# Kernel tuning notes

Hardware: AMD Instinct MI355X
Metric: run time of the kernel (lower is better)

Reference implementation:

```python
import jax, jax.numpy as jnp
import numpy as np

D_MODEL = 1024
Q_DIM = K_DIM = V_DIM = 1024
MASKED = True

def setup_inputs() -> dict:
    key = jax.random.key(0)
    ks = jax.random.split(key, 7)
    s = 1.0 / np.sqrt(D_MODEL)
    return {
        "x": jax.random.normal(ks[0], (4, 2048, D_MODEL), dtype=jnp.float32),
        "Wq": jax.random.uniform(ks[1], (D_MODEL, Q_DIM), jnp.float32, -s, s),
        "bq": jax.random.uniform(ks[2], (Q_DIM,), jnp.float32, -s, s),
        "Wk": jax.random.uniform(ks[3], (D_MODEL, K_DIM), jnp.float32, -s, s),
        "bk": jax.random.uniform(ks[4], (K_DIM,), jnp.float32, -s, s),
        "Wv": jax.random.uniform(ks[5], (D_MODEL, V_DIM), jnp.float32, -s, s),
        "bv": jax.random.uniform(ks[6], (V_DIM,), jnp.float32, -s, s),
    }

def reference(x, Wq, bq, Wk, bk, Wv, bv):
    # QKV projections: [b, s, d]
    q = x @ Wq + bq
    k = x @ Wk + bk
    v = x @ Wv + bv
    dk = k.shape[-1]
    # scores: [b, s_q, s_k]
    scores = jnp.einsum('bqd,bkd->bqk', q, k) / jnp.sqrt(jnp.float32(dk))
    if MASKED:
        s = scores.shape[-1]
        tri = jnp.triu(jnp.ones((s, s), dtype=bool), k=1)  # strictly upper
        scores = jnp.where(tri, jnp.float32(-1e9), scores)
    # NOTE: original softmaxes over dim=-2 (the query axis) — faithful here.
    probs = jax.nn.softmax(scores, axis=-2)
    attn = jnp.einsum('bqk,bkd->bqd', probs, v)
    # dropout in eval mode = identity
    return attn
```

## Files before the change

kernel.cpp:

```cpp
#include <hip/hip_runtime.h>

#define DEV __device__ __forceinline__

typedef float f32x4 __attribute__((ext_vector_type(4)));
typedef short short4v __attribute__((ext_vector_type(4)));
typedef short short8v __attribute__((ext_vector_type(8)));
typedef __bf16 bf16x8 __attribute__((ext_vector_type(8)));

#define QKSTR (2048L * 2048)
#define PSTR  (2048L * 2048)
#define OSTR  (2048L * 1024)

DEV unsigned short f2bf(float f) {
  unsigned int u = __float_as_uint(f);
  u += 0x7fffu + ((u >> 16) & 1u);
  return (unsigned short)(u >> 16);
}
DEV float bf2f(short s) {
  return __uint_as_float(((unsigned int)(unsigned short)s) << 16);
}

DEV void async16(void* lds, const void* g) {
  __builtin_amdgcn_global_load_lds((const __attribute__((address_space(1))) void*)g,
                                   (__attribute__((address_space(3))) void*)lds, 16, 0, 0);
}

DEV void store_elem(float* C, long i, float v) { C[i] = v; }
DEV void store_elem(short* C, long i, float v) { C[i] = (short)f2bf(v); }

__global__ void pre_kernel(const float* __restrict__ x, short* __restrict__ xb,
                           const float* __restrict__ Wq, const float* __restrict__ Wk,
                           const float* __restrict__ Wv, short* __restrict__ wqkt,
                           short* __restrict__ wvt,
                           const float* __restrict__ bq, const float* __restrict__ bk,
                           float* __restrict__ bqk)
{
  __shared__ float t[32][33];
  const int b = blockIdx.x;
  if (b < 4096) {
    long i = ((long)b * 256 + threadIdx.x) * 8;
    f32x4 a = *(const f32x4*)(x + i);
    f32x4 c = *(const f32x4*)(x + i + 4);
    short8v o;
#pragma unroll
    for (int j = 0; j < 4; ++j) { o[j] = (short)f2bf(a[j]); o[4 + j] = (short)f2bf(c[j]); }
    *(short8v*)(xb + i) = o;
  } else if (b < 7168) {
    int tb = b - 4096;
    int which = tb >> 10;
    int t2 = tb & 1023;
    const float* W = (which == 0) ? Wq : (which == 1) ? Wk : Wv;
    short* Wt = (which == 0) ? wqkt : (which == 1) ? (wqkt + 1024 * 1024) : wvt;
    int n0 = (t2 & 31) * 32, k0 = (t2 >> 5) * 32;
    int tx = threadIdx.x & 31, ty = threadIdx.x >> 5;
#pragma unroll
    for (int r = 0; r < 32; r += 8) t[ty + r][tx] = W[(long)(k0 + ty + r) * 1024 + n0 + tx];
    __syncthreads();
#pragma unroll
    for (int r = 0; r < 32; r += 8)
      Wt[(long)(n0 + ty + r) * 1024 + k0 + tx] = (short)f2bf(t[tx][ty + r]);
  } else {
    int i = (b - 7168) * 256 + threadIdx.x;
    bqk[i] = (i < 1024) ? bq[i] : bk[i - 1024];
  }
}

template <typename CT, int MODE>
DEV void gemm_body(short* As0, short* As1, short* Bs0, short* Bs1,
                   const short* A, const short* Bt, CT* C,
                   int K, int lda, int ldbt, int ldc,
                   const float* bias_m, const float* bias_n, float scale,
                   float* ps_out, int bn, int bm, int bz)
{
  const int kend = (MODE == 2) ? min(K, (bm + 1) * 128) : K;

  const int tid = threadIdx.x;
  const int wid = tid >> 6, lane = tid & 63;
  const int wm = wid >> 1, wn = wid & 1;
  const int rC = lane >> 2;
  const int swS = (rC & 3) ^ ((rC >> 2) & 3);
  const int kB = (((lane & 3) ^ swS)) * 8;
  const int fr = lane & 15;
  const int swR = (fr & 3) ^ ((fr >> 2) & 3);
  const int fkB = (((lane >> 4) ^ swR)) * 16;

  const short* Ab = A + (long)bm * 128 * lda + (long)rC * lda + kB;
  const short* Bb = Bt + (long)bn * 128 * ldbt + (long)rC * ldbt + kB;

  f32x4 acc[4][4] = {};

  auto STAGE = [&](short* Asb, short* Bsb, int kk) {
#pragma unroll
    for (int j = 0; j < 2; ++j) {
      int chunk = j * 4 + wid;
      async16(&Asb[chunk * 512], Ab + (long)chunk * 16 * lda + kk);
      async16(&Bsb[chunk * 512], Bb + (long)chunk * 16 * ldbt + kk);
    }
  };

  STAGE(As0, Bs0, 0);
  int cur = 0;
  for (int kk = 0; kk < kend; kk += 32) {
    const short* Ac = cur ? As1 : As0;
    const short* Bc = cur ? Bs1 : Bs0;
    if (kk + 32 < kend) {
      STAGE(cur ? As0 : As1, cur ? Bs0 : Bs1, kk + 32);
      asm volatile("s_waitcnt vmcnt(4)" ::: "memory");
    } else {
      asm volatile("s_waitcnt vmcnt(0)" ::: "memory");
    }
    __builtin_amdgcn_s_barrier();
    __builtin_amdgcn_sched_barrier(0);

    bf16x8 af[4], bf_[4];
#pragma unroll
    for (int i = 0; i < 4; ++i)
      af[i] = *(const bf16x8*)((const char*)Ac + (wm * 64 + i * 16 + fr) * 64 + fkB);
#pragma unroll
    for (int j = 0; j < 4; ++j)
      bf_[j] = *(const bf16x8*)((const char*)Bc + (wn * 64 + j * 16 + fr) * 64 + fkB);
#pragma unroll
    for (int i = 0; i < 4; ++i)
#pragma unroll
      for (int j = 0; j < 4; ++j)
        acc[i][j] = __builtin_amdgcn_mfma_f32_16x16x32_bf16(af[i], bf_[j], acc[i][j], 0, 0, 0);
    __builtin_amdgcn_s_barrier();
    cur ^= 1;
  }

  const int fq = lane >> 4;

  if constexpr (MODE != 1) {
#pragma unroll
    for (int i = 0; i < 4; ++i) {
#pragma unroll
      for (int r = 0; r < 4; ++r) {
        int row = bm * 128 + wm * 64 + i * 16 + fq * 4 + r;
        float bmv = bias_m ? bias_m[row] : 0.f;
#pragma unroll
        for (int j = 0; j < 4; ++j) {
          int col = bn * 128 + wn * 64 + j * 16 + fr;
          float bnv = bias_n ? bias_n[col] : 0.f;
          store_elem(C, (long)row * ldc + col, acc[i][j][r] * scale + bmv + bnv);
        }
      }
    }
  } else {
    float* ssum = (float*)As0;
    const int rbase = bm * 128 + wm * 64 + fq * 4;
#pragma unroll
    for (int j = 0; j < 4; ++j) {
      const int col = bn * 128 + wn * 64 + j * 16 + fr;
      float s = 0.f;
#pragma unroll
      for (int i = 0; i < 4; ++i)
#pragma unroll
        for (int r = 0; r < 4; ++r) {
          int row = rbase + i * 16 + r;
          float e = (row >= col) ? __expf(acc[i][j][r] * scale) : 0.f;
          s += e;
          C[(long)row * ldc + col] = (short)f2bf(e);
        }
      s += __shfl_xor(s, 16);
      s += __shfl_xor(s, 32);
      if (fq == 0) ssum[wm * 128 + wn * 64 + j * 16 + fr] = s;
    }
    __syncthreads();
    if (tid < 128) {
      long o = ((long)bz * 16 + bm) * 2048 + bn * 128 + tid;
      ps_out[o] = ssum[tid] + ssum[128 + tid];
    }
  }
}

template <typename CT, int MODE>
__global__ __launch_bounds__(256, 4) void gemm_bt(
    const short* __restrict__ A, const short* __restrict__ Bt, CT* __restrict__ C,
    int K, int lda, int ldbt, int ldc,
    long sA, long sBt, long sC,
    const float* __restrict__ bias_m, const float* __restrict__ bias_n, float scale)
{
  __shared__ __align__(16) short lds[4][4096];
  int bn, bm;
  if constexpr (MODE == 2) {
    const int k = (int)blockIdx.x;
    const int y = (int)blockIdx.y;
    bm = (y < 8) ? (15 - k) : k;
    bn = y & 7;
  } else {
    const int nwg = (int)(gridDim.x * gridDim.y);
    int L = (int)blockIdx.y * (int)gridDim.x + (int)blockIdx.x;
    if ((nwg & 7) == 0) L = (L & 7) * (nwg >> 3) + (L >> 3);
    bn = L % (int)gridDim.x;
    bm = L / (int)gridDim.x;
  }
  const int bz = blockIdx.z;
  gemm_body<CT, MODE>(lds[0], lds[1], lds[2], lds[3],
                      A + (long)bz * sA, Bt + (long)bz * sBt, C + (long)bz * sC,
                      K, lda, ldbt, ldc, bias_m, bias_n, scale,
                      nullptr, bn, bm, bz);
}

__global__ __launch_bounds__(256, 4) void qkv_proj(
    const short* __restrict__ xb, const short* __restrict__ wqkt,
    const float* __restrict__ bqk, short* __restrict__ qkb,
    const short* __restrict__ wvt, const float* __restrict__ bv,
    short* __restrict__ vt)
{
  __shared__ __align__(16) short lds[4][4096];
  int b = (int)blockIdx.x;
  b = (b & 7) * 192 + (b >> 3);
  const int slice = b / 192;
  const int j = b - slice * 192;
  if (j < 128) {
    const int bn = j >> 3;
    const int bm = slice * 8 + (j & 7);
    gemm_body<short, 0>(lds[0], lds[1], lds[2], lds[3],
                        xb, wqkt, qkb, 1024, 1024, 1024, 2048,
                        nullptr, bqk, 1.f, nullptr, bn, bm, 0);
  } else {
    const int j2 = j - 128;
    const int bm = j2 >> 3;
    const int bn = slice * 8 + (j2 & 7);
    gemm_body<short, 0>(lds[0], lds[1], lds[2], lds[3],
                        wvt, xb, vt, 1024, 1024, 1024, 8192,
                        bv, nullptr, 1.f, nullptr, bn, bm, 0);
  }
}

__global__ __launch_bounds__(256, 4) void scores_k(
    const short* __restrict__ qkb, short* __restrict__ P,
    float* __restrict__ psum, int z0)
{
  __shared__ __align__(16) short lds[4][4096];
  const int nwg = (int)gridDim.x;
  int b = (int)blockIdx.x;
  b = (b & 7) * (nwg >> 3) + (b >> 3);
  const int z = b / 136;
  int idx = b - z * 136;
  int bm = 0;
  while ((bm + 1) * (bm + 2) / 2 <= idx) ++bm;
  int bn = idx - bm * (bm + 1) / 2;
  const long qoff = (long)(z0 + z) * QKSTR;
  gemm_body<short, 1>(lds[0], lds[1], lds[2], lds[3],
                      qkb + qoff, qkb + qoff + 1024, P + (long)z * PSTR,
                      1024, 2048, 2048, 2048, nullptr, nullptr, 0.03125f,
                      psum, bn, bm, z);
}

__global__ __launch_bounds__(256) void vscale_finv(
    const short* __restrict__ vt, const float* __restrict__ psum,
    short* __restrict__ vts, int b0)
{
  const int z = blockIdx.y;
  const int kc = blockIdx.x;
  const int k0 = kc * 32;
  __shared__ float finv[32];
  const int t = threadIdx.x;
  if (t < 32) {
    const int k = k0 + t;
    float D = 0.f;
    for (int ch = k >> 7; ch < 16; ++ch) D += psum[((long)z * 16 + ch) * 2048 + k];
    finv[t] = 1.f / D;
  }
  __syncthreads();
  const int kg = (t & 3) * 8;
  f32x4 fa = *(const f32x4*)(&finv[kg]);
  f32x4 fb = *(const f32x4*)(&finv[kg + 4]);
  const int dbase = t >> 2;
  const short* src = vt + (long)(b0 + z) * 2048 + k0 + kg;
  short* dst = vts + (long)z * 2048 + k0 + kg;
#pragma unroll 4
  for (int pass = 0; pass < 16; ++pass) {
    const long d = dbase + pass * 64;
    short8v v = *(const short8v*)(src + d * 8192);
    short8v o;
#pragma unroll
    for (int j = 0; j < 4; ++j) {
      o[j]     = (short)f2bf(bf2f(v[j]) * fa[j]);
      o[4 + j] = (short)f2bf(bf2f(v[4 + j]) * fb[j]);
    }
    *(short8v*)(dst + d * 8192) = o;
  }
}

extern "C" void kernel_launch(void* const* d_in, const int* in_sizes, int n_in,
                              void* d_out, int out_size, void* d_ws, size_t ws_size,
                              hipStream_t stream) {
  const float* x  = (const float*)d_in[0];
  const float* Wq = (const float*)d_in[1];
  const float* bq = (const float*)d_in[2];
  const float* Wk = (const float*)d_in[3];
  const float* bk = (const float*)d_in[4];
  const float* Wv = (const float*)d_in[5];
  const float* bv = (const float*)d_in[6];
  float* out = (float*)d_out;

  const size_t SZ_XB  = 8192ull * 1024 * 2;
  const size_t SZ_WQK = 2048ull * 1024 * 2;
  const size_t SZ_WT  = 1024ull * 1024 * 2;
  const size_t SZ_QK  = 8192ull * 2048 * 2;
  const size_t SZ_VT  = 1024ull * 8192 * 2;
  const size_t N_PS   = 4ull * 16 * 2048;
  const size_t SZ_STATS = (N_PS + 2048) * 4;
  const size_t SZ_P1 = 2048ull * 2048 * 2;

  char* p = (char*)d_ws;
  short* xb   = (short*)p; p += SZ_XB;
  short* wqkt = (short*)p; p += SZ_WQK;
  short* wvt  = (short*)p; p += SZ_WT;
  short* qkb  = (short*)p; p += SZ_QK;
  short* vt   = (short*)p; p += SZ_VT;
  short* vts  = (short*)p; p += SZ_VT;
  float* psum = (float*)p;
  float* bqk  = psum + N_PS;
  p += SZ_STATS;
  size_t fixed = (size_t)(p - (char*)d_ws);
  int nbuf = (ws_size >= fixed + 4 * SZ_P1) ? 4 : 1;
  short* P = (short*)p;

  pre_kernel<<<dim3(7176), dim3(256), 0, stream>>>(x, xb, Wq, Wk, Wv, wqkt, wvt,
                                                   bq, bk, bqk);

  qkv_proj<<<dim3(1536), dim3(256), 0, stream>>>(xb, wqkt, bqk, qkb, wvt, bv, vt);

  for (int b0 = 0; b0 < 4; b0 += nbuf) {
    const int nz = nbuf;
    scores_k<<<dim3(136 * nz), dim3(256), 0, stream>>>(qkb, P, psum, b0);
    vscale_finv<<<dim3(64, nz), dim3(256), 0, stream>>>(vt, psum, vts, b0);
    gemm_bt<float, 2><<<dim3(8, 16, nz), dim3(256), 0, stream>>>(
        P, vts, out + (long)b0 * OSTR, 2048, 2048, 8192, 1024,
        PSTR, 2048L, OSTR, nullptr, nullptr, 1.f);
  }
}
```

Measured before the change: 164.4 us.

## Fold Q and K projections into a single x·(Wq·Wkᵀ)·xᵀ bilinear form

Rewrites the scores as x·M·xᵀ plus rank-one bias terms. M is a precomputed 1024x1024 product of the Q and K weights, and the per-row bias dot products are folded into the softmax exponent. This replaces the 2048-wide Q/K projection GEMM with a small weight GEMM plus a 1024-wide x·M GEMM, roughly halving projection FLOPs and memory traffic. It adds an extra kernel launch and a dependency stage, and changes rounding because M and y are stored in bf16.

New measurement: 163.4 us. No clear change (-0.6%).

```diff
diff --git a/kernel.cpp b/kernel.cpp
--- a/kernel.cpp
+++ b/kernel.cpp
@@ -7,7 +7,6 @@
 typedef short short8v __attribute__((ext_vector_type(8)));
 typedef __bf16 bf16x8 __attribute__((ext_vector_type(8)));
 
-#define QKSTR (2048L * 2048)
 #define PSTR  (2048L * 2048)
 #define OSTR  (2048L * 1024)
 
@@ -28,40 +27,81 @@
 DEV void store_elem(float* C, long i, float v) { C[i] = v; }
 DEV void store_elem(short* C, long i, float v) { C[i] = (short)f2bf(v); }
 
+DEV float wave_red(float v) {
+#pragma unroll
+  for (int o = 1; o < 64; o <<= 1) v += __shfl_xor(v, o);
+  return v;
+}
+
 __global__ void pre_kernel(const float* __restrict__ x, short* __restrict__ xb,
                            const float* __restrict__ Wq, const float* __restrict__ Wk,
-                           const float* __restrict__ Wv, short* __restrict__ wqkt,
+                           const float* __restrict__ Wv,
+                           short* __restrict__ wqb, short* __restrict__ wkb,
                            short* __restrict__ wvt,
                            const float* __restrict__ bq, const float* __restrict__ bk,
-                           float* __restrict__ bqk)
+                           float* __restrict__ g, float* __restrict__ h,
+                           float* __restrict__ cbuf)
 {
   __shared__ float t[32][33];
   const int b = blockIdx.x;
+  const int tid = threadIdx.x;
   if (b < 4096) {
-    long i = ((long)b * 256 + threadIdx.x) * 8;
+    long i = ((long)b * 256 + tid) * 8;
     f32x4 a = *(const f32x4*)(x + i);
-    f32x4 c = *(const f32x4*)(x + i + 4);
+    f32x4 c2 = *(const f32x4*)(x + i + 4);
     short8v o;
 #pragma unroll
-    for (int j = 0; j < 4; ++j) { o[j] = (short)f2bf(a[j]); o[4 + j] = (short)f2bf(c[j]); }
+    for (int j = 0; j < 4; ++j) { o[j] = (short)f2bf(a[j]); o[4 + j] = (short)f2bf(c2[j]); }
     *(short8v*)(xb + i) = o;
-  } else if (b < 7168) {
+  } else if (b < 5120) {
     int tb = b - 4096;
-    int which = tb >> 10;
-    int t2 = tb & 1023;
-    const float* W = (which == 0) ? Wq : (which == 1) ? Wk : Wv;
-    short* Wt = (which == 0) ? wqkt : (which == 1) ? (wqkt + 1024 * 1024) : wvt;
+    const float* W = (tb < 512) ? Wq : Wk;
+    short* Wo = (tb < 512) ? wqb : wkb;
+    long i = ((long)(tb & 511) * 256 + tid) * 8;
+    f32x4 a = *(const f32x4*)(W + i);
+    f32x4 c2 = *(const f32x4*)(W + i + 4);
+    short8v o;
+#pragma unroll
+    for (int j = 0; j < 4; ++j) { o[j] = (short)f2bf(a[j]); o[4 + j] = (short)f2bf(c2[j]); }
+    *(short8v*)(Wo + i) = o;
+  } else if (b < 6144) {
+    int t2 = b - 5120;
     int n0 = (t2 & 31) * 32, k0 = (t2 >> 5) * 32;
-    int tx = threadIdx.x & 31, ty = threadIdx.x >> 5;
-#pragma unroll
-    for (int r = 0; r < 32; r += 8) t[ty + r][tx] = W[(long)(k0 + ty + r) * 1024 + n0 + tx];
+    int tx = tid & 31, ty = tid >> 5;
+#pragma unroll
+    for (int r = 0; r < 32; r += 8) t[ty + r][tx] = Wv[(long)(k0 + ty + r) * 1024 + n0 + tx];
     __syncthreads();
 #pragma unroll
     for (int r = 0; r < 32; r += 8)
-      Wt[(long)(n0 + ty + r) * 1024 + k0 + tx] = (short)f2bf(t[tx][ty + r]);
+      wvt[(long)(n0 + ty + r) * 1024 + k0 + tx] = (short)f2bf(t[tx][ty + r]);
+  } else if (b < 6656) {
+    int local = b - 6144;
+    const float* W = (local < 256) ? Wq : Wk;
+    const float* bb = (local < 256) ? bk : bq;
+    float* out = (local < 256) ? g : h;
+    const int d = (local & 255) * 4 + (tid >> 6);
+    const int lane = tid & 63;
+    const float* row = W + (long)d * 1024 + lane * 16;
+    const float* bp = bb + lane * 16;
+    float s = 0.f;
+#pragma unroll
+    for (int q = 0; q < 4; ++q) {
+      f32x4 wv = *(const f32x4*)(row + q * 4);
+      f32x4 bv2 = *(const f32x4*)(bp + q * 4);
+#pragma unroll
+      for (int j = 0; j < 4; ++j) s += wv[j] * bv2[j];
+    }
+    s = wave_red(s);
+    if (lane == 0) out[d] = s;
   } else {
-    int i = (b - 7168) * 256 + threadIdx.x;
-    bqk[i] = (i < 1024) ? bq[i] : bk[i - 1024];
+    float s = 0.f;
+#pragma unroll
+    for (int q = 0; q < 4; ++q) s += bq[tid + q * 256] * bk[tid + q * 256];
+    s = wave_red(s);
+    __shared__ float red[4];
+    if ((tid & 63) == 0) red[tid >> 6] = s;
+    __syncthreads();
+    if (tid == 0) cbuf[0] = red[0] + red[1] + red[2] + red[3];
   }
 }
 
@@ -70,6 +110,7 @@
                    const short* A, const short* Bt, CT* C,
                    int K, int lda, int ldbt, int ldc,
                    const float* bias_m, const float* bias_n, float scale,
+                   const float* u_vec, const float* w_vec,
                    float* ps_out, int bn, int bm, int bz)
 {
   const int kend = (MODE == 2) ? min(K, (bm + 1) * 128) : K;
@@ -148,16 +189,22 @@
   } else {
     float* ssum = (float*)As0;
     const int rbase = bm * 128 + wm * 64 + fq * 4;
+    float uu[4][4];
+#pragma unroll
+    for (int i = 0; i < 4; ++i)
+#pragma unroll
+      for (int r = 0; r < 4; ++r) uu[i][r] = u_vec[rbase + i * 16 + r];
 #pragma unroll
     for (int j = 0; j < 4; ++j) {
       const int col = bn * 128 + wn * 64 + j * 16 + fr;
+      const float wc = w_vec[col];
       float s = 0.f;
 #pragma unroll
       for (int i = 0; i < 4; ++i)
 #pragma unroll
         for (int r = 0; r < 4; ++r) {
           int row = rbase + i * 16 + r;
-          float e = (row >= col) ? __expf(acc[i][j][r] * scale) : 0.f;
+          float e = (row >= col) ? __expf((acc[i][j][r] + uu[i][r] + wc) * scale) : 0.f;
           s += e;
           C[(long)row * ldc + col] = (short)f2bf(e);
         }
@@ -181,56 +228,92 @@
     const float* __restrict__ bias_m, const float* __restrict__ bias_n, float scale)
 {
   __shared__ __align__(16) short lds[4][4096];
-  int bn, bm;
-  if constexpr (MODE == 2) {
-    const int k = (int)blockIdx.x;
-    const int y = (int)blockIdx.y;
-    bm = (y < 8) ? (15 - k) : k;
-    bn = y & 7;
-  } else {
-    const int nwg = (int)(gridDim.x * gridDim.y);
-    int L = (int)blockIdx.y * (int)gridDim.x + (int)blockIdx.x;
-    if ((nwg & 7) == 0) L = (L & 7) * (nwg >> 3) + (L >> 3);
-    bn = L % (int)gridDim.x;
-    bm = L / (int)gridDim.x;
-  }
+  const int k = (int)blockIdx.x;
+  const int y = (int)blockIdx.y;
+  const int bm = (y < 8) ? (15 - k) : k;
+  const int bn = y & 7;
   const int bz = blockIdx.z;
   gemm_body<CT, MODE>(lds[0], lds[1], lds[2], lds[3],
                       A + (long)bz * sA, Bt + (long)bz * sBt, C + (long)bz * sC,
                       K, lda, ldbt, ldc, bias_m, bias_n, scale,
-                      nullptr, bn, bm, bz);
-}
-
-__global__ __launch_bounds__(256, 4) void qkv_proj(
-    const short* __restrict__ xb, const short* __restrict__ wqkt,
-    const float* __restrict__ bqk, short* __restrict__ qkb,
-    const short* __restrict__ wvt, const float* __restrict__ bv,
-    short* __restrict__ vt)
+                      nullptr, nullptr, nullptr, bn, bm, bz);
+}
+
+__global__ __launch_bounds__(256, 4) void aux_kernel(
+    const short* __restrict__ wqb, const short* __restrict__ wkb,
+    short* __restrict__ Mt,
+    const short* __restrict__ xb, const short* __restrict__ wvt,
+    const float* __restrict__ bv, short* __restrict__ vt,
+    const float* __restrict__ g, const float* __restrict__ h,
+    const float* __restrict__ cbuf,
+    float* __restrict__ u, float* __restrict__ w)
 {
   __shared__ __align__(16) short lds[4][4096];
   int b = (int)blockIdx.x;
-  b = (b & 7) * 192 + (b >> 3);
-  const int slice = b / 192;
-  const int j = b - slice * 192;
-  if (j < 128) {
-    const int bn = j >> 3;
-    const int bm = slice * 8 + (j & 7);
+  const int k = b & 7;
+  const int j = b >> 3;
+  if (j < 8) {
+    const int id = k * 8 + j;
     gemm_body<short, 0>(lds[0], lds[1], lds[2], lds[3],
-                        xb, wqkt, qkb, 1024, 1024, 1024, 2048,
-                        nullptr, bqk, 1.f, nullptr, bn, bm, 0);
-  } else {
-    const int j2 = j - 128;
+                        wkb, wqb, Mt, 1024, 1024, 1024, 1024,
+                        nullptr, nullptr, 1.f, nullptr, nullptr, nullptr,
+                        id & 7, id >> 3, 0);
+  } else if (j < 72) {
+    const int j2 = j - 8;
+    const int bn = k * 8 + (j2 & 7);
     const int bm = j2 >> 3;
-    const int bn = slice * 8 + (j2 & 7);
     gemm_body<short, 0>(lds[0], lds[1], lds[2], lds[3],
                         wvt, xb, vt, 1024, 1024, 1024, 8192,
-                        bv, nullptr, 1.f, nullptr, bn, bm, 0);
-  }
+                        bv, nullptr, 1.f, nullptr, nullptr, nullptr, bn, bm, 0);
+  } else {
+    const int id = k * 256 + (j - 72);
+    const int wv_ = threadIdx.x >> 6, lane = threadIdx.x & 63;
+    const int s = id * 4 + wv_;
+    const short* row = xb + (long)s * 1024 + lane * 16;
+    const float* gp = g + lane * 16;
+    const float* hp = h + lane * 16;
+    short8v xa = *(const short8v*)(row);
+    short8v xb2 = *(const short8v*)(row + 8);
+    float du = 0.f, dw = 0.f;
+#pragma unroll
+    for (int q = 0; q < 2; ++q) {
+      f32x4 ga = *(const f32x4*)(gp + q * 4);
+      f32x4 gb = *(const f32x4*)(gp + 8 + q * 4);
+      f32x4 ha = *(const f32x4*)(hp + q * 4);
+      f32x4 hb = *(const f32x4*)(hp + 8 + q * 4);
+#pragma unroll
+      for (int i2 = 0; i2 < 4; ++i2) {
+        float xv0 = bf2f(xa[q * 4 + i2]);
+        float xv1 = bf2f(xb2[q * 4 + i2]);
+        du += xv0 * ga[i2] + xv1 * gb[i2];
+        dw += xv0 * ha[i2] + xv1 * hb[i2];
+      }
+    }
+    du = wave_red(du);
+    dw = wave_red(dw);
+    if (lane == 0) { u[s] = du + cbuf[0]; w[s] = dw; }
+  }
+}
+
+__global__ __launch_bounds__(256, 4) void ygemm(
+    const short* __restrict__ xb, const short* __restrict__ Mt,
+    short* __restrict__ y)
+{
+  __shared__ __align__(16) short lds[4][4096];
+  int b = (int)blockIdx.x;
+  const int k = b & 7;
+  const int j = b >> 3;
+  const int bn = j >> 3;
+  const int bm = k * 8 + (j & 7);
+  gemm_body<short, 0>(lds[0], lds[1], lds[2], lds[3],
+                      xb, Mt, y, 1024, 1024, 1024, 1024,
+                      nullptr, nullptr, 1.f, nullptr, nullptr, nullptr, bn, bm, 0);
 }
 
 __global__ __launch_bounds__(256, 4) void scores_k(
-    const short* __restrict__ qkb, short* __restrict__ P,
-    float* __restrict__ psum, int z0)
+    const short* __restrict__ y, const short* __restrict__ xb,
+    short* __restrict__ P, const float* __restrict__ u,
+    const float* __restrict__ w, float* __restrict__ psum, int z0)
 {
   __shared__ __align__(16) short lds[4][4096];
   const int nwg = (int)gridDim.x;
@@ -241,10 +324,11 @@
   int bm = 0;
   while ((bm + 1) * (bm + 2) / 2 <= idx) ++bm;
   int bn = idx - bm * (bm + 1) / 2;
-  const long qoff = (long)(z0 + z) * QKSTR;
+  const long off = (long)(z0 + z) * 2048 * 1024;
   gemm_body<short, 1>(lds[0], lds[1], lds[2], lds[3],
-                      qkb + qoff, qkb + qoff + 1024, P + (long)z * PSTR,
-                      1024, 2048, 2048, 2048, nullptr, nullptr, 0.03125f,
+                      y + off, xb + off, P + (long)z * PSTR,
+                      1024, 1024, 1024, 2048, nullptr, nullptr, 0.03125f,
+                      u + (long)(z0 + z) * 2048, w + (long)(z0 + z) * 2048,
                       psum, bn, bm, z);
 }
 
@@ -297,36 +381,44 @@
   float* out = (float*)d_out;
 
   const size_t SZ_XB  = 8192ull * 1024 * 2;
-  const size_t SZ_WQK = 2048ull * 1024 * 2;
-  const size_t SZ_WT  = 1024ull * 1024 * 2;
-  const size_t SZ_QK  = 8192ull * 2048 * 2;
+  const size_t SZ_W   = 1024ull * 1024 * 2;
   const size_t SZ_VT  = 1024ull * 8192 * 2;
   const size_t N_PS   = 4ull * 16 * 2048;
-  const size_t SZ_STATS = (N_PS + 2048) * 4;
-  const size_t SZ_P1 = 2048ull * 2048 * 2;
+  const size_t SZ_SM  = (N_PS + 8192 * 2 + 1024 * 2 + 64) * 4;
+  const size_t SZ_P1  = 2048ull * 2048 * 2;
 
   char* p = (char*)d_ws;
-  short* xb   = (short*)p; p += SZ_XB;
-  short* wqkt = (short*)p; p += SZ_WQK;
-  short* wvt  = (short*)p; p += SZ_WT;
-  short* qkb  = (short*)p; p += SZ_QK;
-  short* vt   = (short*)p; p += SZ_VT;
-  short* vts  = (short*)p; p += SZ_VT;
+  short* xb  = (short*)p; p += SZ_XB;
+  short* yb  = (short*)p; p += SZ_XB;
+  short* wqb = (short*)p; p += SZ_W;
+  short* wkb = (short*)p; p += SZ_W;
+  short* wvt = (short*)p; p += SZ_W;
+  short* Mt  = (short*)p; p += SZ_W;
+  short* vt  = (short*)p; p += SZ_VT;
+  short* vts = (short*)p; p += SZ_VT;
   float* psum = (float*)p;
-  float* bqk  = psum + N_PS;
-  p += SZ_STATS;
+  float* u    = psum + N_PS;
+  float* w    = u + 8192;
+  float* g    = w + 8192;
+  float* h    = g + 1024;
+  float* cbuf = h + 1024;
+  p += SZ_SM;
   size_t fixed = (size_t)(p - (char*)d_ws);
   int nbuf = (ws_size >= fixed + 4 * SZ_P1) ? 4 : 1;
   short* P = (short*)p;
 
-  pre_kernel<<<dim3(7176), dim3(256), 0, stream>>>(x, xb, Wq, Wk, Wv, wqkt, wvt,
-                                                   bq, bk, bqk);
-
-  qkv_proj<<<dim3(1536), dim3(256), 0, stream>>>(xb, wqkt, bqk, qkb, wvt, bv, vt);
+  pre_kernel<<<dim3(6657), dim3(256), 0, stream>>>(
+      x, xb, Wq, Wk, Wv, wqb, wkb, wvt, bq, bk, g, h, cbuf);
+
+  aux_kernel<<<dim3(2624), dim3(256), 0, stream>>>(
+      wqb, wkb, Mt, xb, wvt, bv, vt, g, h, cbuf, u, w);
+
+  ygemm<<<dim3(512), dim3(256), 0, stream>>>(xb, Mt, yb);
 
   for (int b0 = 0; b0 < 4; b0 += nbuf) {
     const int nz = nbuf;
-    scores_k<<<dim3(136 * nz), dim3(256), 0, stream>>>(qkb, P, psum, b0);
+    scores_k<<<dim3(136 * nz), dim3(256), 0, stream>>>(
+        yb, xb, P, u, w, psum, b0);
     vscale_finv<<<dim3(64, nz), dim3(256), 0, stream>>>(vt, psum, vts, b0);
     gemm_bt<float, 2><<<dim3(8, 16, nz), dim3(256), 0, stream>>>(
         P, vts, out + (long)b0 * OSTR, 2048, 2048, 8192, 1024,
```
